# Performance work log

Hardware: AMD Instinct MI355X
Metric: run time of the kernel (lower is better)

## Reference

```python
import jax, jax.numpy as jnp
import numpy as np

B, S, D = 4, 2048, 1024
H = 16
HD = D // H


def setup_inputs() -> dict:
    key = jax.random.key(0)
    ks = jax.random.split(key, 6)
    s = 1.0 / np.sqrt(D)
    x = jax.random.normal(ks[0], (B, S, D), dtype=jnp.float32)
    Wq = jax.random.uniform(ks[1], (D, D), jnp.float32, -s, s)
    Wk = jax.random.uniform(ks[2], (D, D), jnp.float32, -s, s)
    Wv = jax.random.uniform(ks[3], (D, D), jnp.float32, -s, s)
    Wo = jax.random.uniform(ks[4], (D, D), jnp.float32, -s, s)
    bo = jax.random.uniform(ks[5], (D,), jnp.float32, -s, s)
    return {"x": x, "Wq": Wq, "Wk": Wk, "Wv": Wv, "Wo": Wo, "bo": bo}


def reference(x, Wq, Wk, Wv, Wo, bo):
    b, n, _ = x.shape
    # QKV projections (nn.Linear applies x @ W.T; W here stored as [d_in, d_out])
    q = (x @ Wq).reshape(b, n, H, HD).transpose(0, 2, 1, 3)  # [b,h,s,hd]
    k = (x @ Wk).reshape(b, n, H, HD).transpose(0, 2, 1, 3)
    v = (x @ Wv).reshape(b, n, H, HD).transpose(0, 2, 1, 3)
    scores = jnp.einsum('bhqd,bhkd->bhqk', q, k) / np.sqrt(HD).astype(np.float32)
    causal = jnp.tril(jnp.ones((n, n), dtype=bool))  # True = keep
    scores = jnp.where(causal, scores, -jnp.inf)
    attn = jax.nn.softmax(scores, axis=-1)
    ctx = jnp.einsum('bhqk,bhkd->bhqd', attn, v)  # [b,h,s,hd]
    ctx = ctx.transpose(0, 2, 1, 3).reshape(b, n, D)
    return ctx @ Wo + bo
```

## Files before the change

### kernel.cpp

```cpp
#include <hip/hip_runtime.h>

#define NB 4
#define NS 2048
#define ND 1024
#define NH 16
#define NHD 64
#define NTOK (NB*NS)

typedef float f32x4 __attribute__((ext_vector_type(4)));
typedef __bf16 bf16x8 __attribute__((ext_vector_type(8)));
typedef __bf16 bf16x4 __attribute__((ext_vector_type(4)));

#define MFMA16(a,b,c) __builtin_amdgcn_mfma_f32_16x16x32_bf16((a),(b),(c),0,0,0)
#define SBAR() __builtin_amdgcn_s_barrier()
#define VMCNT(n) asm volatile("s_waitcnt vmcnt(" #n ")" ::: "memory")
#define LGKM(n) asm volatile("s_waitcnt lgkmcnt(" #n ")" ::: "memory")
#define SCHEDB() __builtin_amdgcn_sched_barrier(0)

__device__ __forceinline__ float fexp2(float x) {
#if __has_builtin(__builtin_amdgcn_exp2f)
  return __builtin_amdgcn_exp2f(x);
#else
  return __expf(x * 0.69314718056f);
#endif
}

__device__ __forceinline__ void gload_lds16(const __bf16* g, const __bf16* l) {
  __builtin_amdgcn_global_load_lds(
      (const __attribute__((address_space(1))) void*)(uintptr_t)(const void*)g,
      (__attribute__((address_space(3))) void*)(uint32_t)(uintptr_t)(const void*)l,
      16, 0, 0);
}

__global__ void k_convert_x(const float* __restrict__ x, __bf16* __restrict__ xb) {
  int i = blockIdx.x * blockDim.x + threadIdx.x;
  float4 v = ((const float4*)x)[i];
  bf16x4 o = { (__bf16)v.x, (__bf16)v.y, (__bf16)v.z, (__bf16)v.w };
  ((bf16x4*)xb)[i] = o;
}

__global__ void k_transpose_w(const float* __restrict__ w0, const float* __restrict__ w1,
                              const float* __restrict__ w2, const float* __restrict__ w3,
                              __bf16* __restrict__ wqkvt, __bf16* __restrict__ wot) {
  __shared__ float tl[64][65];
  const int z = blockIdx.z;
  const float* src = (z==0)?w0:(z==1)?w1:(z==2)?w2:w3;
  __bf16* dst = (z<3) ? (wqkvt + (size_t)z*ND*ND) : wot;
  const int kb = blockIdx.x*64, nb = blockIdx.y*64;
  const int c = threadIdx.x & 63, r0 = threadIdx.x >> 6;
  for (int i=0;i<16;i++) { int r = r0*16+i; tl[r][c] = src[(size_t)(kb+r)*ND + nb + c]; }
  __syncthreads();
  for (int i=0;i<16;i++) { int r = r0*16+i; dst[(size_t)(nb+r)*ND + kb + c] = (__bf16)tl[c][r]; }
}

__global__ __launch_bounds__(256, 2) void k_gemm_qkv(
    const __bf16* __restrict__ A, const __bf16* __restrict__ Bt,
    __bf16* __restrict__ qs, __bf16* __restrict__ ks, __bf16* __restrict__ vt) {
  constexpr int BUFE = (256+128)*32;
  __shared__ __align__(16) __bf16 lds[3*BUFE];
  const int tid = threadIdx.x;
  const int wid = tid>>6, lane = tid&63;
  const int wr = wid>>1, wc = wid&1;
  const int lrow = lane&15, lg = lane>>4;
  const int srow4 = lane>>2;
  const int scol  = ((lane&3) ^ ((lane>>3)&3))*8;

  const int id  = blockIdx.x;
  const int xcd = id & 7;
  const int nl  = id >> 3;
  const int st  = nl >> 5;
  const int u   = nl & 31;
  const int bx  = xcd*4 + (u >> 3);
  const int by  = st*8 + (u & 7);
  const int m0 = bx*256, n0 = by*128;

  auto stage = [&](int t, int bsel) {
    __bf16* buf = lds + bsel*BUFE;
    const int k0 = t*32;
    #pragma unroll
    for (int i=0;i<4;i++) {
      int c = wid + i*4;
      gload_lds16(A + (size_t)(m0 + c*16 + srow4)*ND + k0 + scol, buf + c*512);
    }
    #pragma unroll
    for (int i=0;i<2;i++) {
      int c = wid + i*4;
      gload_lds16(Bt + (size_t)(n0 + c*16 + srow4)*ND + k0 + scol, buf + 8192 + c*512);
    }
  };

  const int slot = (lg ^ ((lrow>>1)&3)) << 4;
  const int abase = (wr*128 + lrow)*64 + slot;
  const int bbase = 16384 + (wc*64 + lrow)*64 + slot;

  f32x4 acc[8][4];
  f32x4 zero = {0.f,0.f,0.f,0.f};
  #pragma unroll
  for (int i=0;i<8;i++) for (int j=0;j<4;j++) acc[i][j] = zero;

  stage(0,0);
  stage(1,1);
  for (int t=0; t<32; ++t) {
    if (t < 30) stage(t+2, (t+2)%3);
    if (t < 30)      { VMCNT(12); }
    else if (t == 30){ VMCNT(6);  }
    else             { VMCNT(0);  }
    SBAR();
    const char* L = (const char*)(lds + (t%3)*BUFE);
    bf16x8 bfr[4], af[8];
    #pragma unroll
    for (int cb=0;cb<4;cb++) bfr[cb] = *(const bf16x8*)(L + bbase + cb*1024);
    #pragma unroll
    for (int mf=0;mf<4;mf++) af[mf] = *(const bf16x8*)(L + abase + mf*1024);
    SCHEDB();
    #pragma unroll
    for (int mf=4;mf<8;mf++) af[mf] = *(const bf16x8*)(L + abase + mf*1024);
    LGKM(4);
    SCHEDB();
    __builtin_amdgcn_s_setprio(1);
    #pragma unroll
    for (int mf=0;mf<4;mf++)
      #pragma unroll
      for (int cb=0;cb<4;cb++)
        acc[mf][cb] = MFMA16(af[mf], bfr[cb], acc[mf][cb]);
    __builtin_amdgcn_s_setprio(0);
    LGKM(0);
    SCHEDB();
    __builtin_amdgcn_s_setprio(1);
    #pragma unroll
    for (int mf=4;mf<8;mf++)
      #pragma unroll
      for (int cb=0;cb<4;cb++)
        acc[mf][cb] = MFMA16(af[mf], bfr[cb], acc[mf][cb]);
    __builtin_amdgcn_s_setprio(0);
    SBAR();
  }

  const int which = by >> 3;
  const int h = (by&7)*2 + wc;
  __bf16* ws = lds + wid*8192;
  const int tokbase = m0 + wr*128;
  const int b = tokbase >> 11, s0 = tokbase & 2047;

  if (which < 2) {
    __bf16* dst = which ? ks : qs;
    #pragma unroll
    for (int mf=0;mf<8;mf++)
      #pragma unroll
      for (int cb=0;cb<4;cb++)
        #pragma unroll
        for (int r=0;r<4;r++) {
          int row = mf*16 + lg*4 + r;
          int chunk = (cb*2 + (lrow>>3)) ^ (row&7);
          *(__bf16*)((char*)ws + row*128 + chunk*16 + (lrow&7)*2) = (__bf16)acc[mf][cb][r];
        }
    #pragma unroll
    for (int p=0;p<16;p++) {
      int row = p*8 + (lane>>3);
      int chunk = (lane&7) ^ (row&7);
      bf16x8 v = *(const bf16x8*)((char*)ws + row*128 + chunk*16);
      *(bf16x8*)(dst + ((size_t)(b*NH + h)*NS + s0 + row)*NHD + (lane&7)*8) = v;
    }
  } else {
    #pragma unroll
    for (int mf=0;mf<8;mf++)
      #pragma unroll
      for (int cb=0;cb<4;cb++) {
        bf16x4 pk = { (__bf16)acc[mf][cb][0], (__bf16)acc[mf][cb][1],
                      (__bf16)acc[mf][cb][2], (__bf16)acc[mf][cb][3] };
        int hd = cb*16 + lrow;
        int slotv = (mf*2 + (lg>>1)) ^ (hd&15);
        *(bf16x4*)((char*)ws + hd*256 + slotv*16 + (lg&1)*8) = pk;
      }
    #pragma unroll
    for (int p=0;p<16;p++) {
      int idx = p*64 + lane;
      int hd = idx>>4, c = idx&15;
      bf16x8 v = *(const bf16x8*)((char*)ws + hd*256 + ((c ^ (hd&15)))*16);
      *(bf16x8*)(vt + ((size_t)(b*NH + h)*NHD + hd)*NS + s0 + c*8) = v;
    }
  }
}

__global__ __launch_bounds__(512, 2) void k_gemm_out(
    const __bf16* __restrict__ A, const __bf16* __restrict__ Bt,
    const float* __restrict__ bo, float* __restrict__ out) {
  constexpr int BUFE = (256+128)*64;
  __shared__ __align__(16) __bf16 lds[3*BUFE];
  const int tid = threadIdx.x;
  const int wid = tid>>6, lane = tid&63;
  const int wr = wid>>1, wc = wid&1;
  const int lrow = lane&15, lg = lane>>4;
  const int srow = lane>>3;
  const int scol = ((lane&7) ^ srow)*8;

  const int id  = blockIdx.x;
  const int xcd = id & 7;
  const int nl  = id >> 3;
  const int bx  = xcd*4 + (nl >> 3);
  const int by  = nl & 7;
  const int m0 = bx*256, n0 = by*128;

  auto stage = [&](int t, int bsel) {
    __bf16* buf = lds + bsel*BUFE;
    const int k0 = t*64;
    #pragma unroll
    for (int i=0;i<4;i++) {
      int c = wid + i*8;
      gload_lds16(A + (size_t)(m0 + c*8 + srow)*ND + k0 + scol, buf + c*512);
    }
    #pragma unroll
    for (int i=0;i<2;i++) {
      int c = wid + i*8;
      gload_lds16(Bt + (size_t)(n0 + c*8 + srow)*ND + k0 + scol, buf + 16384 + c*512);
    }
  };

  int kx[8];
  #pragma unroll
  for (int kk=0;kk<8;kk++) kx[kk] = ((kk ^ (lrow&7)) << 4);
  const int abase = (wr*64 + lrow)*128;
  const int bbase = 32768 + (wc*64 + lrow)*128;

  f32x4 acc[4][4];
  f32x4 zero = {0.f,0.f,0.f,0.f};
  #pragma unroll
  for (int i=0;i<4;i++) for (int j=0;j<4;j++) acc[i][j] = zero;

  stage(0,0);
  stage(1,1);
  for (int t=0; t<16; ++t) {
    if (t < 14) stage(t+2, (t+2)%3);
    if (t < 14)      { VMCNT(12); }
    else if (t == 14){ VMCNT(6);  }
    else             { VMCNT(0);  }
    SBAR();
    const char* L = (const char*)(lds + (t%3)*BUFE);
    bf16x8 bfr[4][2], af[4][2];
    #pragma unroll
    for (int cb=0;cb<4;cb++)
      #pragma unroll
      for (int ksi=0;ksi<2;ksi++)
        bfr[cb][ksi] = *(const bf16x8*)(L + bbase + cb*2048 + kx[ksi*4+lg]);
    #pragma unroll
    for (int mf=0;mf<2;mf++)
      #pragma unroll
      for (int ksi=0;ksi<2;ksi++)
        af[mf][ksi] = *(const bf16x8*)(L + abase + mf*2048 + kx[ksi*4+lg]);
    SCHEDB();
    #pragma unroll
    for (int mf=2;mf<4;mf++)
      #pragma unroll
      for (int ksi=0;ksi<2;ksi++)
        af[mf][ksi] = *(const bf16x8*)(L + abase + mf*2048 + kx[ksi*4+lg]);
    LGKM(4);
    SCHEDB();
    __builtin_amdgcn_s_setprio(1);
    #pragma unroll
    for (int mf=0;mf<2;mf++)
      #pragma unroll
      for (int cb=0;cb<4;cb++)
        #pragma unroll
        for (int ksi=0;ksi<2;ksi++)
          acc[mf][cb] = MFMA16(af[mf][ksi], bfr[cb][ksi], acc[mf][cb]);
    __builtin_amdgcn_s_setprio(0);
    LGKM(0);
    SCHEDB();
    __builtin_amdgcn_s_setprio(1);
    #pragma unroll
    for (int mf=2;mf<4;mf++)
      #pragma unroll
      for (int cb=0;cb<4;cb++)
        #pragma unroll
        for (int ksi=0;ksi<2;ksi++)
          acc[mf][cb] = MFMA16(af[mf][ksi], bfr[cb][ksi], acc[mf][cb]);
    __builtin_amdgcn_s_setprio(0);
    SBAR();
  }

  #pragma unroll
  for (int cb=0;cb<4;cb++) {
    const int n = n0 + wc*64 + cb*16 + lrow;
    const float bias = bo[n];
    #pragma unroll
    for (int mf=0;mf<4;mf++)
      #pragma unroll
      for (int r=0;r<4;r++) {
        const int m = m0 + wr*64 + mf*16 + lg*4 + r;
        out[(size_t)m*ND + n] = acc[mf][cb][r] + bias;
      }
  }
}

__global__ __launch_bounds__(256, 3) void k_attn(
    const __bf16* __restrict__ qs, const __bf16* __restrict__ ks,
    const __bf16* __restrict__ vt, __bf16* __restrict__ ctx) {
  __shared__ __align__(16) __bf16 sK[2][64*64];
  __shared__ __align__(16) __bf16 sV[2][64*64];
  __shared__ __align__(16) __bf16 sP[4][32*72];
  const int tid = threadIdx.x, w = tid >> 6, lane = tid & 63;
  const int lrow = lane & 15, lg = lane >> 4;
  const int bh = blockIdx.x;
  const int bq = 15 - blockIdx.y;
  const int nt = 2*bq + 2;
  const size_t base = (size_t)bh * NS * NHD;
  const __bf16* Kg = ks + base;
  const __bf16* Vg = vt + base;
  __bf16* sPw = sP[w];

  const int q0w = bq*128 + w*32;
  bf16x8 qf[2][2];
  for (int rb=0;rb<2;rb++)
    for (int kk=0;kk<2;kk++) {
      bf16x8 v = *(const bf16x8*)(qs + base + (size_t)(q0w + rb*16 + lrow)*NHD + kk*32 + lg*8);
      bf16x8 o;
      for (int j=0;j<8;j++) o[j] = (__bf16)((float)v[j] * 0.1803368801f);
      qf[rb][kk] = o;
    }

  int koffB[4][2];
  for (int cb=0;cb<4;cb++) {
    int r = cb*16 + lrow;
    for (int kk=0;kk<2;kk++)
      koffB[cb][kk] = r*128 + (((kk*4 + lg) ^ (r & 7)) << 4);
  }
  const int s_r[2]  = { (w + 0)*8 + (lane>>3), (w + 4)*8 + (lane>>3) };
  const int s_u[2]  = { (lane&7) ^ (s_r[0]&7), (lane&7) ^ (s_r[1]&7) };

  f32x4 zero = {0.f,0.f,0.f,0.f};
  f32x4 oacc[2][4];
  float psum[2] = {0.f, 0.f};
  for (int rb=0;rb<2;rb++) for(int cb=0;cb<4;cb++) oacc[rb][cb]=zero;

  for (int i=0;i<2;i++) {
    gload_lds16(Kg + (size_t)s_r[i]*NHD + s_u[i]*8,              sK[0] + (w + i*4)*512);
    gload_lds16(Vg + (size_t)s_r[i]*NS  + s_u[i]*8,              sV[0] + (w + i*4)*512);
  }
  asm volatile("s_waitcnt vmcnt(0)" ::: "memory");
  __syncthreads();

  int buf = 0;
  for (int t = 0; t < nt; ++t) {
    if (t+1 < nt) {
      const __bf16* Kt = Kg + (size_t)(t+1)*64*NHD;
      for (int i=0;i<2;i++) {
        gload_lds16(Kt + (size_t)s_r[i]*NHD + s_u[i]*8,          sK[buf^1] + (w + i*4)*512);
        gload_lds16(Vg + (size_t)s_r[i]*NS + (t+1)*64 + s_u[i]*8, sV[buf^1] + (w + i*4)*512);
      }
    }
    if (!(t == nt-1 && w < 2)) {
      const __bf16* bK = sK[buf];
      const __bf16* bV = sV[buf];
      const bool bdry = (t >= nt-2);
      for (int cb=0;cb<4;cb++) {
        bf16x8 kf0 = *(const bf16x8*)((const char*)bK + koffB[cb][0]);
        bf16x8 kf1 = *(const bf16x8*)((const char*)bK + koffB[cb][1]);
        const int kvb = t*64 + cb*16 + lg*4;
        for (int rb=0;rb<2;rb++) {
          f32x4 s4 = MFMA16(kf0, qf[rb][0], zero);
          s4 = MFMA16(kf1, qf[rb][1], s4);
          const int qg = q0w + rb*16 + lrow;
          float e0 = fexp2(s4[0]), e1 = fexp2(s4[1]);
          float e2 = fexp2(s4[2]), e3 = fexp2(s4[3]);
          if (bdry) {
            if (kvb + 0 > qg) e0 = 0.f;
            if (kvb + 1 > qg) e1 = 0.f;
            if (kvb + 2 > qg) e2 = 0.f;
            if (kvb + 3 > qg) e3 = 0.f;
          }
          psum[rb] += (e0 + e1) + (e2 + e3);
          bf16x4 pk = { (__bf16)e0, (__bf16)e1, (__bf16)e2, (__bf16)e3 };
          *(bf16x4*)(sPw + (rb*16 + lrow)*72 + cb*16 + lg*4) = pk;
        }
      }
      for (int kk=0;kk<2;kk++) {
        bf16x8 pa0 = *(const bf16x8*)(sPw + (lrow)*72      + kk*32 + lg*8);
        bf16x8 pa1 = *(const bf16x8*)(sPw + (16 + lrow)*72 + kk*32 + lg*8);
        for (int cb=0;cb<4;cb++) {
          bf16x8 vb = *(const bf16x8*)((const char*)bV + koffB[cb][kk]);
          oacc[0][cb] = MFMA16(pa0, vb, oacc[0][cb]);
          oacc[1][cb] = MFMA16(pa1, vb, oacc[1][cb]);
        }
      }
    }
    asm volatile("s_waitcnt vmcnt(0)" ::: "memory");
    __syncthreads();
    buf ^= 1;
  }

  float inv[2];
  for (int rb=0;rb<2;rb++) {
    float s = psum[rb];
    s += __shfl_xor(s, 16);
    s += __shfl_xor(s, 32);
    inv[rb] = 1.0f / s;
  }

  __bf16* ws = &sK[0][0] + w*2048;
  const int b = bh >> 4, h = bh & 15;
  for (int rb=0;rb<2;rb++)
    for (int cb=0;cb<4;cb++)
      for (int r=0;r<4;r++) {
        int row = rb*16 + lg*4 + r;
        float nrm = __shfl(inv[rb], lg*4 + r);
        int chunk = (cb*2 + (lrow>>3)) ^ (row&7);
        *(__bf16*)((char*)ws + row*128 + chunk*16 + (lrow&7)*2) =
            (__bf16)(oacc[rb][cb][r] * nrm);
      }
  for (int p=0;p<4;p++) {
    int row = p*8 + (lane>>3);
    int chunk = (lane&7) ^ (row&7);
    bf16x8 v = *(const bf16x8*)((char*)ws + row*128 + chunk*16);
    int q = q0w + row;
    *(bf16x8*)(ctx + ((size_t)(b*NS + q))*ND + h*NHD + (lane&7)*8) = v;
  }
}

extern "C" void kernel_launch(void* const* d_in, const int* in_sizes, int n_in,
                              void* d_out, int out_size, void* d_ws, size_t ws_size,
                              hipStream_t stream) {
  const float* x  = (const float*)d_in[0];
  const float* Wq = (const float*)d_in[1];
  const float* Wk = (const float*)d_in[2];
  const float* Wv = (const float*)d_in[3];
  const float* Wo = (const float*)d_in[4];
  const float* bo = (const float*)d_in[5];
  float* out = (float*)d_out;

  __bf16* xb    = (__bf16*)d_ws;
  __bf16* wqkvt = xb    + (size_t)NTOK*ND;
  __bf16* wot   = wqkvt + (size_t)3*ND*ND;
  __bf16* qsc   = wot   + (size_t)ND*ND;
  __bf16* ksc   = qsc   + (size_t)NTOK*ND;
  __bf16* vtc   = ksc   + (size_t)NTOK*ND;
  __bf16* ctx   = vtc   + (size_t)NTOK*ND;

  k_convert_x<<<NTOK*ND/(4*256), 256, 0, stream>>>(x, xb);
  k_transpose_w<<<dim3(ND/64, ND/64, 4), 256, 0, stream>>>(Wq, Wk, Wv, Wo, wqkvt, wot);
  k_gemm_qkv<<<768, 256, 0, stream>>>(xb, wqkvt, qsc, ksc, vtc);
  k_attn<<<dim3(NB*NH, NS/128), 256, 0, stream>>>(qsc, ksc, vtc, ctx);
  k_gemm_out<<<256, 512, 0, stream>>>(ctx, wot, bo, out);
}
```

Measured before the change: 144.1 us.

## Merge prep kernels and load V fragments directly from global in attention

Fuses the x conversion and weight transpose into one launch to save a kernel launch. In attention, V tiles are no longer staged through LDS; each lane reads its V^T fragments straight from global memory into registers, which frees LDS. Launch bounds are raised from 3 to 4 blocks per CU. This risks exposed global latency on V loads and more register pressure, since the V loads are issued at the start of each iteration without a prefetch.

```diff
diff --git a/kernel.cpp b/kernel.cpp
--- a/kernel.cpp
+++ b/kernel.cpp
@@ -32,25 +32,28 @@
       16, 0, 0);
 }
 
-__global__ void k_convert_x(const float* __restrict__ x, __bf16* __restrict__ xb) {
-  int i = blockIdx.x * blockDim.x + threadIdx.x;
-  float4 v = ((const float4*)x)[i];
-  bf16x4 o = { (__bf16)v.x, (__bf16)v.y, (__bf16)v.z, (__bf16)v.w };
-  ((bf16x4*)xb)[i] = o;
-}
-
-__global__ void k_transpose_w(const float* __restrict__ w0, const float* __restrict__ w1,
-                              const float* __restrict__ w2, const float* __restrict__ w3,
-                              __bf16* __restrict__ wqkvt, __bf16* __restrict__ wot) {
+__global__ void k_prep(const float* __restrict__ x,
+                       const float* __restrict__ w0, const float* __restrict__ w1,
+                       const float* __restrict__ w2, const float* __restrict__ w3,
+                       __bf16* __restrict__ xb, __bf16* __restrict__ wqkvt,
+                       __bf16* __restrict__ wot) {
   __shared__ float tl[64][65];
-  const int z = blockIdx.z;
-  const float* src = (z==0)?w0:(z==1)?w1:(z==2)?w2:w3;
-  __bf16* dst = (z<3) ? (wqkvt + (size_t)z*ND*ND) : wot;
-  const int kb = blockIdx.x*64, nb = blockIdx.y*64;
-  const int c = threadIdx.x & 63, r0 = threadIdx.x >> 6;
-  for (int i=0;i<16;i++) { int r = r0*16+i; tl[r][c] = src[(size_t)(kb+r)*ND + nb + c]; }
-  __syncthreads();
-  for (int i=0;i<16;i++) { int r = r0*16+i; dst[(size_t)(nb+r)*ND + kb + c] = (__bf16)tl[c][r]; }
+  const int bi = blockIdx.x;
+  if (bi < 1024) {
+    const int z = bi >> 8, rem = bi & 255;
+    const float* src = (z==0)?w0:(z==1)?w1:(z==2)?w2:w3;
+    __bf16* dst = (z<3) ? (wqkvt + (size_t)z*ND*ND) : wot;
+    const int kb = (rem>>4)*64, nb = (rem&15)*64;
+    const int c = threadIdx.x & 63, r0 = threadIdx.x >> 6;
+    for (int i=0;i<16;i++) { int r = r0*16+i; tl[r][c] = src[(size_t)(kb+r)*ND + nb + c]; }
+    __syncthreads();
+    for (int i=0;i<16;i++) { int r = r0*16+i; dst[(size_t)(nb+r)*ND + kb + c] = (__bf16)tl[c][r]; }
+  } else {
+    const int i = (bi - 1024)*256 + threadIdx.x;
+    float4 v = ((const float4*)x)[i];
+    bf16x4 o = { (__bf16)v.x, (__bf16)v.y, (__bf16)v.z, (__bf16)v.w };
+    ((bf16x4*)xb)[i] = o;
+  }
 }
 
 __global__ __launch_bounds__(256, 2) void k_gemm_qkv(
@@ -292,11 +295,10 @@
   }
 }
 
-__global__ __launch_bounds__(256, 3) void k_attn(
+__global__ __launch_bounds__(256, 4) void k_attn(
     const __bf16* __restrict__ qs, const __bf16* __restrict__ ks,
     const __bf16* __restrict__ vt, __bf16* __restrict__ ctx) {
   __shared__ __align__(16) __bf16 sK[2][64*64];
-  __shared__ __align__(16) __bf16 sV[2][64*64];
   __shared__ __align__(16) __bf16 sP[4][32*72];
   const int tid = threadIdx.x, w = tid >> 6, lane = tid & 63;
   const int lrow = lane & 15, lg = lane >> 4;
@@ -324,6 +326,11 @@
     for (int kk=0;kk<2;kk++)
       koffB[cb][kk] = r*128 + (((kk*4 + lg) ^ (r & 7)) << 4);
   }
+  const __bf16* vb8[2][4];
+  for (int kk=0;kk<2;kk++)
+    for (int cb=0;cb<4;cb++)
+      vb8[kk][cb] = Vg + (size_t)(cb*16 + lrow)*NS + kk*32 + lg*8;
+
   const int s_r[2]  = { (w + 0)*8 + (lane>>3), (w + 4)*8 + (lane>>3) };
   const int s_u[2]  = { (lane&7) ^ (s_r[0]&7), (lane&7) ^ (s_r[1]&7) };
 
@@ -332,25 +339,29 @@
   float psum[2] = {0.f, 0.f};
   for (int rb=0;rb<2;rb++) for(int cb=0;cb<4;cb++) oacc[rb][cb]=zero;
 
-  for (int i=0;i<2;i++) {
-    gload_lds16(Kg + (size_t)s_r[i]*NHD + s_u[i]*8,              sK[0] + (w + i*4)*512);
-    gload_lds16(Vg + (size_t)s_r[i]*NS  + s_u[i]*8,              sV[0] + (w + i*4)*512);
-  }
+  for (int i=0;i<2;i++)
+    gload_lds16(Kg + (size_t)s_r[i]*NHD + s_u[i]*8, sK[0] + (w + i*4)*512);
   asm volatile("s_waitcnt vmcnt(0)" ::: "memory");
   __syncthreads();
 
   int buf = 0;
   for (int t = 0; t < nt; ++t) {
+    const bool compute = !(t == nt-1 && w < 2);
+    bf16x8 vf[2][4];
+    if (compute) {
+      #pragma unroll
+      for (int kk=0;kk<2;kk++)
+        #pragma unroll
+        for (int cb=0;cb<4;cb++)
+          vf[kk][cb] = *(const bf16x8*)(vb8[kk][cb] + t*64);
+    }
     if (t+1 < nt) {
       const __bf16* Kt = Kg + (size_t)(t+1)*64*NHD;
-      for (int i=0;i<2;i++) {
-        gload_lds16(Kt + (size_t)s_r[i]*NHD + s_u[i]*8,          sK[buf^1] + (w + i*4)*512);
-        gload_lds16(Vg + (size_t)s_r[i]*NS + (t+1)*64 + s_u[i]*8, sV[buf^1] + (w + i*4)*512);
-      }
-    }
-    if (!(t == nt-1 && w < 2)) {
+      for (int i=0;i<2;i++)
+        gload_lds16(Kt + (size_t)s_r[i]*NHD + s_u[i]*8, sK[buf^1] + (w + i*4)*512);
+    }
+    if (compute) {
       const __bf16* bK = sK[buf];
-      const __bf16* bV = sV[buf];
       const bool bdry = (t >= nt-2);
       for (int cb=0;cb<4;cb++) {
         bf16x8 kf0 = *(const bf16x8*)((const char*)bK + koffB[cb][0]);
@@ -377,9 +388,8 @@
         bf16x8 pa0 = *(const bf16x8*)(sPw + (lrow)*72      + kk*32 + lg*8);
         bf16x8 pa1 = *(const bf16x8*)(sPw + (16 + lrow)*72 + kk*32 + lg*8);
         for (int cb=0;cb<4;cb++) {
-          bf16x8 vb = *(const bf16x8*)((const char*)bV + koffB[cb][kk]);
-          oacc[0][cb] = MFMA16(pa0, vb, oacc[0][cb]);
-          oacc[1][cb] = MFMA16(pa1, vb, oacc[1][cb]);
+          oacc[0][cb] = MFMA16(pa0, vf[kk][cb], oacc[0][cb]);
+          oacc[1][cb] = MFMA16(pa1, vf[kk][cb], oacc[1][cb]);
         }
       }
     }
@@ -435,8 +445,7 @@
   __bf16* vtc   = ksc   + (size_t)NTOK*ND;
   __bf16* ctx   = vtc   + (size_t)NTOK*ND;
 
-  k_convert_x<<<NTOK*ND/(4*256), 256, 0, stream>>>(x, xb);
-  k_transpose_w<<<dim3(ND/64, ND/64, 4), 256, 0, stream>>>(Wq, Wk, Wv, Wo, wqkvt, wot);
+  k_prep<<<1024 + NTOK*ND/(4*256), 256, 0, stream>>>(x, Wq, Wk, Wv, Wo, xb, wqkvt, wot);
   k_gemm_qkv<<<768, 256, 0, stream>>>(xb, wqkvt, qsc, ksc, vtc);
   k_attn<<<dim3(NB*NH, NS/128), 256, 0, stream>>>(qsc, ksc, vtc, ctx);
   k_gemm_out<<<256, 512, 0, stream>>>(ctx, wot, bo, out);
```

Result: slower. 244.1 us (+69.4%).
